# Kernel tuning notes

Measured on AMD Instinct MI355X. Metric: run time of the kernel, lower is better.

The kernel has to match this reference:

```python
import jax, jax.numpy as jnp
import numpy as np

D_MODEL = 1024
D_HID = D_MODEL // 4
N_EXPERTS = 64
TOP_K = 2


def setup_inputs() -> dict:
    key = jax.random.key(0)
    k_x, k_w1, k_b1, k_w2, k_b2 = jax.random.split(key, 5)
    # torch Linear default init: U(-1/sqrt(fan_in), 1/sqrt(fan_in))
    s1 = 1.0 / np.sqrt(D_MODEL)
    s2 = 1.0 / np.sqrt(D_HID)
    return {
        "x": jax.random.normal(k_x, (4, 4096, D_MODEL), dtype=jnp.float32),
        "W1": jax.random.uniform(k_w1, (D_MODEL, D_HID), jnp.float32, -s1, s1),
        "b1": jax.random.uniform(k_b1, (D_HID,), jnp.float32, -s1, s1),
        "W2": jax.random.uniform(k_w2, (D_HID, N_EXPERTS), jnp.float32, -s2, s2),
        "b2": jax.random.uniform(k_b2, (N_EXPERTS,), jnp.float32, -s2, s2),
    }


def reference(x, W1, b1, W2, b2):
    # gate MLP: [B,S,D] -> [B,S,H] -> tanh -> [B,S,E]
    h = jnp.tanh(jnp.einsum("bsd,dh->bsh", x, W1) + b1)
    gate_logits = jnp.einsum("bsh,he->bse", h, W2) + b2
    # top-k selection + softmax over the k selected logits
    top_logits, top_idx = jax.lax.top_k(gate_logits, TOP_K)  # [B,S,K]
    top_gates = jax.nn.softmax(top_logits, axis=-1)          # [B,S,K]
    # scatter back into dense [B,S,E] gate tensor
    onehot = jax.nn.one_hot(top_idx, N_EXPERTS, dtype=top_gates.dtype)  # [B,S,K,E]
    gates = jnp.einsum("bsk,bske->bse", top_gates, onehot)
    return gates, gate_logits
```

## Files before the change

### kernel.cpp

```cpp
#include <hip/hip_runtime.h>
#include <math.h>


#define DM 1024
#define DH 256
#define NE 64

#define W1P_OFF 0
#define W1P_STRIDE 524288
#define W2P_OFF 1572864
#define W2P_STRIDE 32768

#define HSTR 276
#define AROW 80
#define APLANE 5120
#define ABUF 15360
#define SMEM_BYTES 70656

typedef __attribute__((ext_vector_type(8))) short bf16x8;
typedef __attribute__((ext_vector_type(4))) float f32x4;

__device__ __forceinline__ unsigned fbits(float f) { return __float_as_uint(f); }
__device__ __forceinline__ float topf(unsigned u) { return __uint_as_float(u & 0xFFFF0000u); }

__device__ __forceinline__ void split3(float v, unsigned& h, unsigned& m, unsigned& l) {
    h = fbits(v);
    float r1 = v - topf(h);
    m = fbits(r1);
    float r2 = r1 - topf(m);
    l = fbits(r2);
}
__device__ __forceinline__ unsigned packpair(unsigned a, unsigned b) {
    return (a >> 16) | (b & 0xFFFF0000u);
}
__device__ __forceinline__ bf16x8 as_bf(uint4 u) {
    union { uint4 a; bf16x8 b; } c; c.a = u; return c.b;
}

__device__ __forceinline__ void stage4(float4 f, char* wb) {
    unsigned h[4], m[4], l[4];
    split3(f.x, h[0], m[0], l[0]);
    split3(f.y, h[1], m[1], l[1]);
    split3(f.z, h[2], m[2], l[2]);
    split3(f.w, h[3], m[3], l[3]);
    uint2 dh = {packpair(h[0], h[1]), packpair(h[2], h[3])};
    uint2 dm = {packpair(m[0], m[1]), packpair(m[2], m[3])};
    uint2 dl = {packpair(l[0], l[1]), packpair(l[2], l[3])};
    *(uint2*)(wb + 0 * APLANE) = dh;
    *(uint2*)(wb + 1 * APLANE) = dm;
    *(uint2*)(wb + 2 * APLANE) = dl;
}

__device__ __forceinline__ void split_pack8(float4 f0, float4 f1,
                                            bf16x8& H, bf16x8& M, bf16x8& L) {
    float v[8] = {f0.x, f0.y, f0.z, f0.w, f1.x, f1.y, f1.z, f1.w};
    unsigned hb[8], mb[8], lb[8];
#pragma unroll
    for (int j = 0; j < 8; j++) split3(v[j], hb[j], mb[j], lb[j]);
    uint4 uh = {packpair(hb[0], hb[1]), packpair(hb[2], hb[3]),
                packpair(hb[4], hb[5]), packpair(hb[6], hb[7])};
    uint4 um = {packpair(mb[0], mb[1]), packpair(mb[2], mb[3]),
                packpair(mb[4], mb[5]), packpair(mb[6], mb[7])};
    uint4 ul = {packpair(lb[0], lb[1]), packpair(lb[2], lb[3]),
                packpair(lb[4], lb[5]), packpair(lb[6], lb[7])};
    H = as_bf(uh); M = as_bf(um); L = as_bf(ul);
}


__global__ __launch_bounds__(256)
void prep_planes(const float* __restrict__ W1, const float* __restrict__ W2,
                 char* __restrict__ ws) {
    __shared__ float tile[512];
    unsigned* w1p = (unsigned*)(ws + W1P_OFF);
    unsigned* w2p = (unsigned*)(ws + W2P_OFF);
    const int b = blockIdx.x, t = threadIdx.x;
    const int q = t & 3, L = (t >> 2) & 63;
    const int n_loc = L & 15;
    const int k_loc = ((L >> 4) & 3) * 8 + 2 * q;
    if (b < 512) {
        const int kc = b >> 4, nt = b & 15;
#pragma unroll
        for (int i = 0; i < 2; i++) {
            const int idx = t + i * 256;
            tile[idx] = W1[(size_t)(kc * 32 + (idx >> 4)) * DH + nt * 16 + (idx & 15)];
        }
        __syncthreads();
        const float v0 = tile[k_loc * 16 + n_loc];
        const float v1 = tile[(k_loc + 1) * 16 + n_loc];
        unsigned h0, m0, l0, h1, m1, l1;
        split3(v0, h0, m0, l0);
        split3(v1, h1, m1, l1);
        const int gt = b * 256 + t;
        w1p[0 * 131072 + gt] = packpair(h0, h1);
        w1p[1 * 131072 + gt] = packpair(m0, m1);
        w1p[2 * 131072 + gt] = packpair(l0, l1);
    } else {
        const int b2 = b - 512;
        const int kc = b2 >> 2, nt = b2 & 3;
#pragma unroll
        for (int i = 0; i < 2; i++) {
            const int idx = t + i * 256;
            tile[idx] = W2[(kc * 32 + (idx >> 4)) * NE + nt * 16 + (idx & 15)];
        }
        __syncthreads();
        const float v0 = tile[k_loc * 16 + n_loc];
        const float v1 = tile[(k_loc + 1) * 16 + n_loc];
        unsigned h0, m0, l0, h1, m1, l1;
        split3(v0, h0, m0, l0);
        split3(v1, h1, m1, l1);
        const int g2 = b2 * 256 + t;
        w2p[0 * 8192 + g2] = packpair(h0, h1);
        w2p[1 * 8192 + g2] = packpair(m0, m1);
        w2p[2 * 8192 + g2] = packpair(l0, l1);
    }
}

__global__ __launch_bounds__(512, 2)
void fused_gating(const float* __restrict__ x, const char* __restrict__ w1p,
                  const float* __restrict__ b1, const char* __restrict__ w2p,
                  const float* __restrict__ b2, float* __restrict__ gates,
                  float* __restrict__ logits_out) {
    __shared__ __align__(16) char smem[SMEM_BYTES];
    char* alds = smem;
    float* hlds = (float*)smem;

    const int tid  = threadIdx.x;
    const int lane = tid & 63;
    const int wave = tid >> 6;
    const int m15 = lane & 15;
    const int lq  = lane >> 4;
    const int t0 = blockIdx.x * 64;

    const int stok = tid >> 3;
    const int seg  = tid & 7;
    const float* xs = x + (size_t)(t0 + stok) * DM + seg * 4;
    const int swoff = stok * AROW + seg * 8;

    const char* bbase = w1p + (size_t)(wave * 2) * 1024 + lane * 16;

    f32x4 acc[4][2];
#pragma unroll
    for (int ms = 0; ms < 4; ms++)
#pragma unroll
        for (int nt = 0; nt < 2; nt++) acc[ms][nt] = (f32x4){0.f, 0.f, 0.f, 0.f};

    stage4(*(const float4*)(xs), alds + swoff);
    float4 xc  = *(const float4*)(xs + 32);
    float4 xc2 = *(const float4*)(xs + 64);
    __syncthreads();

#pragma unroll 2
    for (int kc = 0; kc < 32; kc++) {
        uint4 bc[3][2];
#pragma unroll
        for (int p = 0; p < 3; p++)
#pragma unroll
            for (int nt = 0; nt < 2; nt++)
                bc[p][nt] = *(const uint4*)(bbase + p * W1P_STRIDE + kc * 16384 + nt * 1024);
        float4 xn = *(const float4*)(xs + ((kc + 3) & 31) * 32);

        if (kc < 31)
            stage4(xc, alds + ((kc + 1) & 1) * ABUF + swoff);
        xc = xc2; xc2 = xn;

        const char* ab = alds + (kc & 1) * ABUF + m15 * AROW + lq * 16;
        bf16x8 af[4][3];
#pragma unroll
        for (int ms = 0; ms < 4; ms++)
#pragma unroll
            for (int p = 0; p < 3; p++)
                af[ms][p] = *(const bf16x8*)(ab + p * APLANE + ms * (16 * AROW));

#pragma unroll
        for (int ms = 0; ms < 4; ms++)
#pragma unroll
            for (int nt = 0; nt < 2; nt++) {
                const bf16x8 ah = af[ms][0];
                const bf16x8 am = af[ms][1];
                const bf16x8 al = af[ms][2];
                const bf16x8 bh = as_bf(bc[0][nt]);
                const bf16x8 bm = as_bf(bc[1][nt]);
                const bf16x8 bl = as_bf(bc[2][nt]);
                f32x4 a = acc[ms][nt];
                a = __builtin_amdgcn_mfma_f32_16x16x32_bf16(ah, bh, a, 0, 0, 0);
                a = __builtin_amdgcn_mfma_f32_16x16x32_bf16(ah, bm, a, 0, 0, 0);
                a = __builtin_amdgcn_mfma_f32_16x16x32_bf16(am, bh, a, 0, 0, 0);
                a = __builtin_amdgcn_mfma_f32_16x16x32_bf16(ah, bl, a, 0, 0, 0);
                a = __builtin_amdgcn_mfma_f32_16x16x32_bf16(al, bh, a, 0, 0, 0);
                a = __builtin_amdgcn_mfma_f32_16x16x32_bf16(am, bm, a, 0, 0, 0);
                acc[ms][nt] = a;
            }

        __syncthreads();
    }

#pragma unroll
    for (int nt = 0; nt < 2; nt++) {
        const int hid = wave * 32 + nt * 16 + m15;
        const float bias = b1[hid];
#pragma unroll
        for (int ms = 0; ms < 4; ms++) {
            const int tb = ms * 16 + lq * 4;
#pragma unroll
            for (int r = 0; r < 4; r++)
                hlds[(tb + r) * HSTR + hid] = tanhf(acc[ms][nt][r] + bias);
        }
    }
    __syncthreads();

    if (wave < 4) {
        const float* hb = hlds + (wave * 16 + m15) * HSTR + lq * 8;
        const char* bt = w2p + lane * 16;

        f32x4 gacc[4];
#pragma unroll
        for (int nt = 0; nt < 4; nt++) gacc[nt] = (f32x4){0.f, 0.f, 0.f, 0.f};

#pragma unroll
        for (int kc = 0; kc < 8; kc++) {
            float4 f0 = *(const float4*)(hb + kc * 32);
            float4 f1 = *(const float4*)(hb + kc * 32 + 4);
            bf16x8 afh, afm, afl;
            split_pack8(f0, f1, afh, afm, afl);
#pragma unroll
            for (int nt = 0; nt < 4; nt++) {
                const char* tb = bt + (kc * 4 + nt) * 1024;
                bf16x8 bh = *(const bf16x8*)(tb + 0 * W2P_STRIDE);
                bf16x8 bm = *(const bf16x8*)(tb + 1 * W2P_STRIDE);
                bf16x8 bl = *(const bf16x8*)(tb + 2 * W2P_STRIDE);
                f32x4 a = gacc[nt];
                a = __builtin_amdgcn_mfma_f32_16x16x32_bf16(afh, bh, a, 0, 0, 0);
                a = __builtin_amdgcn_mfma_f32_16x16x32_bf16(afh, bm, a, 0, 0, 0);
                a = __builtin_amdgcn_mfma_f32_16x16x32_bf16(afm, bh, a, 0, 0, 0);
                a = __builtin_amdgcn_mfma_f32_16x16x32_bf16(afh, bl, a, 0, 0, 0);
                a = __builtin_amdgcn_mfma_f32_16x16x32_bf16(afl, bh, a, 0, 0, 0);
                a = __builtin_amdgcn_mfma_f32_16x16x32_bf16(afm, bm, a, 0, 0, 0);
                gacc[nt] = a;
            }
        }

        float b2v[4];
#pragma unroll
        for (int nt = 0; nt < 4; nt++) b2v[nt] = b2[nt * 16 + m15];

#pragma unroll
        for (int r = 0; r < 4; r++) {
            float v[4]; int e[4];
#pragma unroll
            for (int nt = 0; nt < 4; nt++) { v[nt] = gacc[nt][r] + b2v[nt]; e[nt] = nt * 16 + m15; }

            float a1 = v[0], a2 = v[1]; int j1 = e[0], j2 = e[1];
            if (v[1] > v[0]) { a1 = v[1]; j1 = e[1]; a2 = v[0]; j2 = e[0]; }
#pragma unroll
            for (int tt = 2; tt < 4; tt++) {
                if (v[tt] > a1) { a2 = a1; j2 = j1; a1 = v[tt]; j1 = e[tt]; }
                else if (v[tt] > a2) { a2 = v[tt]; j2 = e[tt]; }
            }
#pragma unroll
            for (int off = 1; off < 16; off <<= 1) {
                float ob1 = __shfl_xor(a1, off, 64); int oj1 = __shfl_xor(j1, off, 64);
                float ob2 = __shfl_xor(a2, off, 64); int oj2 = __shfl_xor(j2, off, 64);
                bool bw = (ob1 > a1) || (ob1 == a1 && oj1 < j1);
                float w1v = bw ? ob1 : a1; int w1i = bw ? oj1 : j1;
                float lv = bw ? a1 : ob1;  int li  = bw ? j1 : oj1;
                float rv = bw ? ob2 : a2;  int ri  = bw ? oj2 : j2;
                bool cw = (lv > rv) || (lv == rv && li < ri);
                a1 = w1v; j1 = w1i;
                a2 = cw ? lv : rv; j2 = cw ? li : ri;
            }
            float ex = __expf(a2 - a1);
            float inv = 1.f / (1.f + ex);
            float g1 = inv, g2 = ex * inv;

            const size_t row = (size_t)(t0 + wave * 16 + lq * 4 + r) * NE;
#pragma unroll
            for (int nt = 0; nt < 4; nt++) {
                float gv = (e[nt] == j1) ? g1 : ((e[nt] == j2) ? g2 : 0.f);
                gates[row + e[nt]] = gv;
                logits_out[row + e[nt]] = v[nt];
            }
        }
    }
}

extern "C" void kernel_launch(void* const* d_in, const int* in_sizes, int n_in,
                              void* d_out, int out_size, void* d_ws, size_t ws_size,
                              hipStream_t stream) {
    const float* x  = (const float*)d_in[0];
    const float* W1 = (const float*)d_in[1];
    const float* b1 = (const float*)d_in[2];
    const float* W2 = (const float*)d_in[3];
    const float* b2 = (const float*)d_in[4];

    const int T = in_sizes[0] / DM;
    char* ws = (char*)d_ws;
    float* gates  = (float*)d_out;
    float* logits = (float*)d_out + (size_t)T * NE;

    prep_planes<<<512 + 32, 256, 0, stream>>>(W1, W2, ws);
    fused_gating<<<T / 64, 512, 0, stream>>>(x, ws + W1P_OFF, b1, ws + W2P_OFF, b2,
                                             gates, logits);
}
```

Baseline: 145.7 us.

## Split fused gating block into producer waves staging x and MFMA consumer waves

Adds four producer waves per block (768 threads) that load x rows, split them into bf16 hi/mid/lo planes and stage them into LDS. The eight original waves now only load W1 planes and issue MFMAs, with raised scheduling priority during the MFMA section. The goal is to take the global x loads and the split arithmetic off the MFMA waves so that staging overlaps with compute. In exchange the block is larger, which may lower occupancy or raise register pressure, and the per-iteration barrier still couples the two groups.

```diff
diff --git a/kernel.cpp b/kernel.cpp
--- a/kernel.cpp
+++ b/kernel.cpp
@@ -37,18 +37,20 @@
     union { uint4 a; bf16x8 b; } c; c.a = u; return c.b;
 }
 
-__device__ __forceinline__ void stage4(float4 f, char* wb) {
-    unsigned h[4], m[4], l[4];
-    split3(f.x, h[0], m[0], l[0]);
-    split3(f.y, h[1], m[1], l[1]);
-    split3(f.z, h[2], m[2], l[2]);
-    split3(f.w, h[3], m[3], l[3]);
-    uint2 dh = {packpair(h[0], h[1]), packpair(h[2], h[3])};
-    uint2 dm = {packpair(m[0], m[1]), packpair(m[2], m[3])};
-    uint2 dl = {packpair(l[0], l[1]), packpair(l[2], l[3])};
-    *(uint2*)(wb + 0 * APLANE) = dh;
-    *(uint2*)(wb + 1 * APLANE) = dm;
-    *(uint2*)(wb + 2 * APLANE) = dl;
+__device__ __forceinline__ void stage8s(float4 f0, float4 f1, char* wb) {
+    float v[8] = {f0.x, f0.y, f0.z, f0.w, f1.x, f1.y, f1.z, f1.w};
+    unsigned hb[8], mb[8], lb[8];
+#pragma unroll
+    for (int j = 0; j < 8; j++) split3(v[j], hb[j], mb[j], lb[j]);
+    uint4 uh = {packpair(hb[0], hb[1]), packpair(hb[2], hb[3]),
+                packpair(hb[4], hb[5]), packpair(hb[6], hb[7])};
+    uint4 um = {packpair(mb[0], mb[1]), packpair(mb[2], mb[3]),
+                packpair(mb[4], mb[5]), packpair(mb[6], mb[7])};
+    uint4 ul = {packpair(lb[0], lb[1]), packpair(lb[2], lb[3]),
+                packpair(lb[4], lb[5]), packpair(lb[6], lb[7])};
+    *(uint4*)(wb + 0 * APLANE) = uh;
+    *(uint4*)(wb + 1 * APLANE) = um;
+    *(uint4*)(wb + 2 * APLANE) = ul;
 }
 
 __device__ __forceinline__ void split_pack8(float4 f0, float4 f1,
@@ -115,7 +117,7 @@
     }
 }
 
-__global__ __launch_bounds__(512, 2)
+__global__ __launch_bounds__(768, 2)
 void fused_gating(const float* __restrict__ x, const char* __restrict__ w1p,
                   const float* __restrict__ b1, const char* __restrict__ w2p,
                   const float* __restrict__ b2, float* __restrict__ gates,
@@ -127,83 +129,99 @@
     const int tid  = threadIdx.x;
     const int lane = tid & 63;
     const int wave = tid >> 6;
+    const bool producer = (wave >= 8);
     const int m15 = lane & 15;
     const int lq  = lane >> 4;
     const int t0 = blockIdx.x * 64;
 
-    const int stok = tid >> 3;
-    const int seg  = tid & 7;
-    const float* xs = x + (size_t)(t0 + stok) * DM + seg * 4;
-    const int swoff = stok * AROW + seg * 8;
+    const float* xs = nullptr;
+    int swoff = 0;
+    float4 xc0, xc1, xc20, xc21;
+    if (producer) {
+        const int pt = tid - 512;
+        const int stok = pt >> 2;
+        const int seg  = pt & 3;
+        xs = x + (size_t)(t0 + stok) * DM + seg * 8;
+        swoff = stok * AROW + seg * 16;
+        stage8s(*(const float4*)(xs), *(const float4*)(xs + 4), alds + swoff);
+        xc0  = *(const float4*)(xs + 32);
+        xc1  = *(const float4*)(xs + 36);
+        xc20 = *(const float4*)(xs + 64);
+        xc21 = *(const float4*)(xs + 68);
+    }
 
     const char* bbase = w1p + (size_t)(wave * 2) * 1024 + lane * 16;
-
     f32x4 acc[4][2];
 #pragma unroll
     for (int ms = 0; ms < 4; ms++)
 #pragma unroll
         for (int nt = 0; nt < 2; nt++) acc[ms][nt] = (f32x4){0.f, 0.f, 0.f, 0.f};
 
-    stage4(*(const float4*)(xs), alds + swoff);
-    float4 xc  = *(const float4*)(xs + 32);
-    float4 xc2 = *(const float4*)(xs + 64);
     __syncthreads();
 
-#pragma unroll 2
     for (int kc = 0; kc < 32; kc++) {
-        uint4 bc[3][2];
-#pragma unroll
-        for (int p = 0; p < 3; p++)
-#pragma unroll
-            for (int nt = 0; nt < 2; nt++)
-                bc[p][nt] = *(const uint4*)(bbase + p * W1P_STRIDE + kc * 16384 + nt * 1024);
-        float4 xn = *(const float4*)(xs + ((kc + 3) & 31) * 32);
-
-        if (kc < 31)
-            stage4(xc, alds + ((kc + 1) & 1) * ABUF + swoff);
-        xc = xc2; xc2 = xn;
-
-        const char* ab = alds + (kc & 1) * ABUF + m15 * AROW + lq * 16;
-        bf16x8 af[4][3];
-#pragma unroll
-        for (int ms = 0; ms < 4; ms++)
+        if (producer) {
+            if (kc < 31) {
+                const int kn = (kc + 3) & 31;
+                float4 xn0 = *(const float4*)(xs + kn * 32);
+                float4 xn1 = *(const float4*)(xs + kn * 32 + 4);
+                stage8s(xc0, xc1, alds + ((kc + 1) & 1) * ABUF + swoff);
+                xc0 = xc20; xc1 = xc21;
+                xc20 = xn0; xc21 = xn1;
+            }
+        } else {
+            uint4 bc[3][2];
 #pragma unroll
             for (int p = 0; p < 3; p++)
-                af[ms][p] = *(const bf16x8*)(ab + p * APLANE + ms * (16 * AROW));
-
-#pragma unroll
-        for (int ms = 0; ms < 4; ms++)
-#pragma unroll
-            for (int nt = 0; nt < 2; nt++) {
-                const bf16x8 ah = af[ms][0];
-                const bf16x8 am = af[ms][1];
-                const bf16x8 al = af[ms][2];
-                const bf16x8 bh = as_bf(bc[0][nt]);
-                const bf16x8 bm = as_bf(bc[1][nt]);
-                const bf16x8 bl = as_bf(bc[2][nt]);
-                f32x4 a = acc[ms][nt];
-                a = __builtin_amdgcn_mfma_f32_16x16x32_bf16(ah, bh, a, 0, 0, 0);
-                a = __builtin_amdgcn_mfma_f32_16x16x32_bf16(ah, bm, a, 0, 0, 0);
-                a = __builtin_amdgcn_mfma_f32_16x16x32_bf16(am, bh, a, 0, 0, 0);
-                a = __builtin_amdgcn_mfma_f32_16x16x32_bf16(ah, bl, a, 0, 0, 0);
-                a = __builtin_amdgcn_mfma_f32_16x16x32_bf16(al, bh, a, 0, 0, 0);
-                a = __builtin_amdgcn_mfma_f32_16x16x32_bf16(am, bm, a, 0, 0, 0);
-                acc[ms][nt] = a;
-            }
-
+#pragma unroll
+                for (int nt = 0; nt < 2; nt++)
+                    bc[p][nt] = *(const uint4*)(bbase + p * W1P_STRIDE + kc * 16384 + nt * 1024);
+
+            const char* ab = alds + (kc & 1) * ABUF + m15 * AROW + lq * 16;
+            bf16x8 af[4][3];
+#pragma unroll
+            for (int ms = 0; ms < 4; ms++)
+#pragma unroll
+                for (int p = 0; p < 3; p++)
+                    af[ms][p] = *(const bf16x8*)(ab + p * APLANE + ms * (16 * AROW));
+
+            __builtin_amdgcn_s_setprio(1);
+#pragma unroll
+            for (int ms = 0; ms < 4; ms++)
+#pragma unroll
+                for (int nt = 0; nt < 2; nt++) {
+                    const bf16x8 ah = af[ms][0];
+                    const bf16x8 am = af[ms][1];
+                    const bf16x8 al = af[ms][2];
+                    const bf16x8 bh = as_bf(bc[0][nt]);
+                    const bf16x8 bm = as_bf(bc[1][nt]);
+                    const bf16x8 bl = as_bf(bc[2][nt]);
+                    f32x4 a = acc[ms][nt];
+                    a = __builtin_amdgcn_mfma_f32_16x16x32_bf16(ah, bh, a, 0, 0, 0);
+                    a = __builtin_amdgcn_mfma_f32_16x16x32_bf16(ah, bm, a, 0, 0, 0);
+                    a = __builtin_amdgcn_mfma_f32_16x16x32_bf16(am, bh, a, 0, 0, 0);
+                    a = __builtin_amdgcn_mfma_f32_16x16x32_bf16(ah, bl, a, 0, 0, 0);
+                    a = __builtin_amdgcn_mfma_f32_16x16x32_bf16(al, bh, a, 0, 0, 0);
+                    a = __builtin_amdgcn_mfma_f32_16x16x32_bf16(am, bm, a, 0, 0, 0);
+                    acc[ms][nt] = a;
+                }
+            __builtin_amdgcn_s_setprio(0);
+        }
         __syncthreads();
     }
 
-#pragma unroll
-    for (int nt = 0; nt < 2; nt++) {
-        const int hid = wave * 32 + nt * 16 + m15;
-        const float bias = b1[hid];
-#pragma unroll
-        for (int ms = 0; ms < 4; ms++) {
-            const int tb = ms * 16 + lq * 4;
-#pragma unroll
-            for (int r = 0; r < 4; r++)
-                hlds[(tb + r) * HSTR + hid] = tanhf(acc[ms][nt][r] + bias);
+    if (!producer) {
+#pragma unroll
+        for (int nt = 0; nt < 2; nt++) {
+            const int hid = wave * 32 + nt * 16 + m15;
+            const float bias = b1[hid];
+#pragma unroll
+            for (int ms = 0; ms < 4; ms++) {
+                const int tb = ms * 16 + lq * 4;
+#pragma unroll
+                for (int r = 0; r < 4; r++)
+                    hlds[(tb + r) * HSTR + hid] = tanhf(acc[ms][nt][r] + bias);
+            }
         }
     }
     __syncthreads();
@@ -298,6 +316,6 @@
     float* logits = (float*)d_out + (size_t)T * NE;
 
     prep_planes<<<512 + 32, 256, 0, stream>>>(W1, W2, ws);
-    fused_gating<<<T / 64, 512, 0, stream>>>(x, ws + W1P_OFF, b1, ws + W2P_OFF, b2,
+    fused_gating<<<T / 64, 768, 0, stream>>>(x, ws + W1P_OFF, b1, ws + W2P_OFF, b2,
                                              gates, logits);
 }
```

After: 145.4 us. No clear change (-0.2%).
